# Kernel optimization log

Hardware: AMD Instinct MI355X
Metric: run time of the kernel (lower is better)

Reference implementation:

```python
import jax, jax.numpy as jnp
import numpy as np


def setup_inputs() -> dict:
    key = jax.random.key(0)
    k1, k2 = jax.random.split(key)
    x = jax.random.normal(k1, (16384, 2048), dtype=jnp.float32)
    diag_elements = jax.random.normal(k2, (2048,), dtype=jnp.float32)
    return {"x": x, "diag_elements": diag_elements}


def reference(x, diag_elements):
    # Original: jnp.dot(x, jnp.diag(diag_elements)).
    # Mathematically identical to scaling each column of x by the
    # corresponding diagonal element (broadcast multiply).
    return x * diag_elements
```

## Files before the change

### kernel.cpp

```cpp
#include <hip/hip_runtime.h>

using f4 = __attribute__((ext_vector_type(4))) float;

__global__ __launch_bounds__(256) void DiagonalDense_kernel(
    const f4* __restrict__ x,
    const f4* __restrict__ diag,
    f4* __restrict__ out,
    int n4) {
    const int i0     = blockIdx.x * blockDim.x + threadIdx.x;
    const int stride = gridDim.x * blockDim.x;

    const f4 dv = diag[i0 & 511];

    #pragma unroll 4
    for (int i = i0; i < n4; i += stride) {
        f4 xv = x[i];
        out[i] = xv * dv;
    }
}

extern "C" void kernel_launch(void* const* d_in, const int* in_sizes, int n_in,
                              void* d_out, int out_size, void* d_ws, size_t ws_size,
                              hipStream_t stream) {
    const f4* x    = (const f4*)d_in[0];
    const f4* diag = (const f4*)d_in[1];
    f4* out        = (f4*)d_out;

    const int n  = out_size;
    const int n4 = n / 4;

    const int block = 256;
    const int grid  = 2048;
    DiagonalDense_kernel<<<grid, block, 0, stream>>>(x, diag, out, n4);
}
```

Baseline: 237.2 us.

## Replace grid-stride loop with one tile per block and batched loads

Each block now handles a fixed tile of 8 vectors per thread. All 8 loads are issued before any store, which raises memory-level parallelism, and the grid-stride loop is dropped in favour of launching one block per tile (4096 blocks). The two diagonal vectors are loaded once and alternated by row parity. The kernel assumes the element count divides evenly into tiles and that there are 2048 columns, and it has no bounds check.

```diff
diff --git a/kernel.cpp b/kernel.cpp
--- a/kernel.cpp
+++ b/kernel.cpp
@@ -2,21 +2,28 @@
 
 using f4 = __attribute__((ext_vector_type(4))) float;
 
-__global__ __launch_bounds__(256) void DiagonalDense_kernel(
+constexpr int BLOCK = 256;
+constexpr int K     = 8;
+constexpr int TILE  = BLOCK * K;
+
+__global__ __launch_bounds__(BLOCK) void DiagonalDense_kernel(
     const f4* __restrict__ x,
     const f4* __restrict__ diag,
-    f4* __restrict__ out,
-    int n4) {
-    const int i0     = blockIdx.x * blockDim.x + threadIdx.x;
-    const int stride = gridDim.x * blockDim.x;
+    f4* __restrict__ out) {
+    const int t    = threadIdx.x;
+    const int base = blockIdx.x * TILE;
 
-    const f4 dv = diag[i0 & 511];
+    const f4 dv0 = diag[t];
+    const f4 dv1 = diag[t + 256];
 
-    #pragma unroll 4
-    for (int i = i0; i < n4; i += stride) {
-        f4 xv = x[i];
-        out[i] = xv * dv;
-    }
+    f4 r[K];
+    #pragma unroll
+    for (int j = 0; j < K; ++j)
+        r[j] = x[base + j * BLOCK + t];
+
+    #pragma unroll
+    for (int j = 0; j < K; ++j)
+        out[base + j * BLOCK + t] = r[j] * ((j & 1) ? dv1 : dv0);
 }
 
 extern "C" void kernel_launch(void* const* d_in, const int* in_sizes, int n_in,
@@ -28,8 +35,7 @@
 
     const int n  = out_size;
     const int n4 = n / 4;
+    const int grid = n4 / TILE;
 
-    const int block = 256;
-    const int grid  = 2048;
-    DiagonalDense_kernel<<<grid, block, 0, stream>>>(x, diag, out, n4);
+    DiagonalDense_kernel<<<grid, BLOCK, 0, stream>>>(x, diag, out);
 }
```

Result: faster. 230.0 us (-3.0%).
